# Optimization experiments

Hardware: AMD Instinct MI355X
Metric: run time of the kernel (lower is better)

Reference implementation:

```python
import jax, jax.numpy as jnp
import numpy as np

# Dims: B=4, T=4096, D=4096, G=1, C=4, K=128, I=4 (I2=2), M=32
B, T, D = 4, 4096, 4096
G, C, K, M = 1, 4, 128, 32
I = 4  # 2*dynamic_hidden_dim
EPS = 1e-6


def setup_inputs() -> dict:
    key = jax.random.key(0)
    k1, k2, k3, k4 = jax.random.split(key, 4)
    query_vec = jax.random.normal(k1, (B, T, D), dtype=jnp.float32)
    dw1 = jax.random.normal(k2, (D, G, C, K), dtype=jnp.float32) * 0.02
    qkw = jax.random.normal(k3, (G, C, K, I, M), dtype=jnp.float32) * 0.02
    dd_w = jax.random.normal(k4, (D, G, M * C), dtype=jnp.float32) * 0.02
    return {"query_vec": query_vec, "dw1": dw1, "qkw": qkw, "dd_w": dd_w}


def _rmsnorm_noscale(x):
    var = jnp.mean(jnp.square(x), axis=-1, keepdims=True)
    return x * jax.lax.rsqrt(var + EPS)


def reference(query_vec, dw1, qkw, dd_w):
    # dw_hidden: [B,T,G,C,K]
    dw_hidden = jnp.einsum('btd,dgck->btgck', query_vec, dw1)
    dw_hidden = jax.nn.gelu(dw_hidden, approximate=False)  # torch nn.GELU() = exact erf
    # w: [B,T,G,C,I,M]; split along I into w1,w2 of [B,T,G,C,I/2,M]
    w = jnp.einsum('btgck,gckim->btgcim', dw_hidden, qkw)
    w1, w2 = jnp.split(w, 2, axis=-2)
    w1 = _rmsnorm_noscale(w1)
    # unbind along C=4: order is (pre_q, pre_k, post_q, post_k)
    pre_qw1, pre_kw1, post_qw1, post_kw1 = (w1[:, :, :, i] for i in range(4))
    pre_qw2, pre_kw2, post_qw2, post_kw2 = (w2[:, :, :, i] for i in range(4))
    # dd: [B,T,G,4M] -> tanh -> split into 4 of [B,T,G,M]
    dd = jnp.tanh(jnp.einsum('btd,dgm->btgm', query_vec, dd_w))
    pre_qdd, pre_kdd, post_qdd, post_kdd = jnp.split(dd, 4, axis=-1)
    # gen_cache=True path: KW [B,T,2,M,M]
    eye = jnp.eye(M, dtype=query_vec.dtype)
    pre_kw = jnp.einsum('bsgim,bsgin->bsmn', pre_kw1, pre_kw2) + pre_kdd[:, :, 0, :, None] * eye
    post_kw = jnp.einsum('bsgim,bsgin->bsmn', post_kw1, post_kw2) + post_kdd[:, :, 0, :, None] * eye
    KW = jnp.stack((pre_kw, post_kw), axis=-3)
    return (pre_qw1, pre_qw2, pre_kw1, pre_kw2, pre_qdd, pre_kdd,
            post_qw1, post_qw2, post_kw1, post_kw2, post_qdd, post_kdd, KW)
```

## Files before the change

kernel.cpp:

```cpp
#include <hip/hip_runtime.h>
#include <hip/hip_bf16.h>


typedef _Float16 half8 __attribute__((ext_vector_type(8)));
typedef float f32x4 __attribute__((ext_vector_type(4)));

#define BT_TOK 16384
#define DDIM   4096

static constexpr int OFF_PRE_QW1  = 0;
static constexpr int OFF_PRE_QW2  = 1048576;
static constexpr int OFF_PRE_KW1  = 2097152;
static constexpr int OFF_PRE_KW2  = 3145728;
static constexpr int OFF_PRE_QDD  = 4194304;
static constexpr int OFF_PRE_KDD  = 4718592;
static constexpr int OFF_POST_QW1 = 5242880;
static constexpr int OFF_POST_QW2 = 6291456;
static constexpr int OFF_POST_KW1 = 7340032;
static constexpr int OFF_POST_KW2 = 8388608;
static constexpr int OFF_POST_QDD = 9437184;
static constexpr int OFF_POST_KDD = 9961472;
static constexpr int OFF_KW       = 10485760;

typedef __attribute__((address_space(3))) void lds_void;
typedef const __attribute__((address_space(1))) void gbl_void;

__device__ __forceinline__ void gload16(const void* g, void* l) {
  __builtin_amdgcn_global_load_lds((gbl_void*)g, (lds_void*)l, 16, 0, 0);
}

__global__ __launch_bounds__(256) void convert_a(const float* __restrict__ q,
                                                 _Float16* __restrict__ a) {
  const int stride = gridDim.x * blockDim.x;
  for (int i = blockIdx.x * blockDim.x + threadIdx.x; i < (BT_TOK * DDIM) / 8;
       i += stride) {
    const float4* p = (const float4*)(q + (size_t)i * 8);
    float4 x = p[0], y = p[1];
    half8 h;
    h[0] = (_Float16)x.x; h[1] = (_Float16)x.y;
    h[2] = (_Float16)x.z; h[3] = (_Float16)x.w;
    h[4] = (_Float16)y.x; h[5] = (_Float16)y.y;
    h[6] = (_Float16)y.z; h[7] = (_Float16)y.w;
    *(half8*)(a + (size_t)i * 8) = h;
  }
}

__global__ __launch_bounds__(256) void build_bt(const float* __restrict__ dw1,
                                                const float* __restrict__ ddw,
                                                _Float16* __restrict__ Bt) {
  __shared__ float tile[64][65];
  const int bn = blockIdx.x % 10, bd = blockIdx.x / 10;
  const int n0 = bn * 64, d0 = bd * 64;
  const int tid = threadIdx.x;
  const int ln = tid & 63;
  const int rr = tid >> 6;
#pragma unroll
  for (int i = 0; i < 16; ++i) {
    int dl = rr + i * 4;
    int d = d0 + dl, n = n0 + ln;
    float v = (n < 512) ? dw1[d * 512 + n] : ddw[d * 128 + (n - 512)];
    tile[dl][ln] = v;
  }
  __syncthreads();
#pragma unroll
  for (int i = 0; i < 16; ++i) {
    int nl = rr + i * 4;
    Bt[(size_t)(n0 + nl) * DDIM + d0 + ln] = (_Float16)tile[ln][nl];
  }
}

__global__ __launch_bounds__(256) void build_qkwT(const float* __restrict__ qkw,
                                                  _Float16* __restrict__ qT) {
  __shared__ float t[128][129];
  const int c = blockIdx.x;
  const float* src = qkw + c * 16384;
  for (int z = threadIdx.x; z < 16384; z += 256) {
    int k = z >> 7, n = z & 127;
    t[k][n] = src[z];
  }
  __syncthreads();
  for (int z = threadIdx.x; z < 16384; z += 256) {
    int n = z >> 7, k = z & 127;
    qT[c * 16384 + z] = (_Float16)t[k][n];
  }
}

__global__ __launch_bounds__(256) void gemm_main(const _Float16* __restrict__ A,
                                                 const _Float16* __restrict__ Bt,
                                                 _Float16* __restrict__ Hg,
                                                 float* __restrict__ out) {
  __shared__ _Float16 As[2][8192];
  __shared__ _Float16 Bs[2][8192];

  int wg = (int)blockIdx.x;
  wg = (wg & 7) * 80 + (wg >> 3);
  const int mtile = wg / 5, ntile = wg - mtile * 5;
  const int m0 = mtile << 7, n0 = ntile << 7;

  const int tid = threadIdx.x;
  const int wave = tid >> 6, lane = tid & 63;
  const int lq = lane >> 4, lc = lane & 15;

  int aoff[4], boff[4], lbase[4];
#pragma unroll
  for (int j = 0; j < 4; ++j) {
    int slot = j * 256 + wave * 64 + lane;
    int row = slot >> 3;
    int gs = (slot & 7) ^ (row & 7);
    aoff[j] = (m0 + row) * DDIM + gs * 8;
    boff[j] = (n0 + row) * DDIM + gs * 8;
    lbase[j] = j * 2048 + wave * 512;
  }
  const int wm = (wave >> 1) << 6, wn = (wave & 1) << 6;

  f32x4 acc[4][4];
#pragma unroll
  for (int i = 0; i < 4; ++i)
#pragma unroll
    for (int j = 0; j < 4; ++j) acc[i][j] = f32x4{0.f, 0.f, 0.f, 0.f};

  auto stage = [&](int b, int k0) {
#pragma unroll
    for (int j = 0; j < 4; ++j) gload16(A + aoff[j] + k0, &As[b][lbase[j]]);
#pragma unroll
    for (int j = 0; j < 4; ++j) gload16(Bt + boff[j] + k0, &Bs[b][lbase[j]]);
  };

  auto compute = [&](int b) {
#pragma unroll
    for (int kk = 0; kk < 2; ++kk) {
      half8 af[4], bf[4];
      const int kb = kk * 4 + lq;
#pragma unroll
      for (int f = 0; f < 4; ++f) {
        int rowA = wm + f * 16 + lc;
        af[f] = *(const half8*)(&As[b][rowA * 64 + ((kb ^ (rowA & 7)) << 3)]);
        int rowB = wn + f * 16 + lc;
        bf[f] = *(const half8*)(&Bs[b][rowB * 64 + ((kb ^ (rowB & 7)) << 3)]);
      }
#pragma unroll
      for (int mf = 0; mf < 4; ++mf)
#pragma unroll
        for (int nf = 0; nf < 4; ++nf)
          acc[mf][nf] = __builtin_amdgcn_mfma_f32_16x16x32_f16(
              af[mf], bf[nf], acc[mf][nf], 0, 0, 0);
    }
  };

  stage(0, 0);
  __syncthreads();
  for (int t = 0; t < 63; ++t) {
    stage((t + 1) & 1, (t + 1) << 6);
    compute(t & 1);
    __syncthreads();
  }
  compute(1);

  if (ntile < 4) {
#pragma unroll
    for (int mf = 0; mf < 4; ++mf)
#pragma unroll
      for (int nf = 0; nf < 4; ++nf)
#pragma unroll
        for (int r = 0; r < 4; ++r) {
          int row = m0 + wm + mf * 16 + lq * 4 + r;
          int col = n0 + wn + nf * 16 + lc;
          float v = acc[mf][nf][r];
          float g = 0.5f * v * (1.0f + erff(v * 0.70710678118654752f));
          Hg[(size_t)row * 512 + col] = (_Float16)g;
        }
  } else {
#pragma unroll
    for (int mf = 0; mf < 4; ++mf)
#pragma unroll
      for (int nf = 0; nf < 4; ++nf)
#pragma unroll
        for (int r = 0; r < 4; ++r) {
          int row = m0 + wm + mf * 16 + lq * 4 + r;
          int j = wn + nf * 16 + lc;
          int t = j >> 5;
          int base = (t & 2) ? ((t & 1) ? OFF_POST_KDD : OFF_POST_QDD)
                             : ((t & 1) ? OFF_PRE_KDD : OFF_PRE_QDD);
          out[base + row * 32 + (j & 31)] = tanhf(acc[mf][nf][r]);
        }
  }
}

__global__ __launch_bounds__(256) void epilogue_k(const _Float16* __restrict__ Hg,
                                                  const _Float16* __restrict__ qT,
                                                  float* __restrict__ out) {
  __shared__ _Float16 hga[16][520];
  __shared__ float stash[2][4][16][32];
  __shared__ float ddl[2][16][32];
  const int tid = threadIdx.x;
  const int wave = tid >> 6, lane = tid & 63;
  const int lq = lane >> 4, lc = lane & 15;
  const int tok0 = blockIdx.x * 16;
  const int c = wave;

#pragma unroll
  for (int z = 0; z < 4; ++z) {
    int flat = z * 256 + tid;
    int row = flat >> 6, c16 = flat & 63;
    *(half8*)(&hga[row][c16 * 8]) =
        *(const half8*)(Hg + (size_t)(tok0 + row) * 512 + c16 * 8);
  }

#pragma unroll
  for (int z = 0; z < 4; ++z) {
    int idx = z * 256 + tid;
    int pp = idx >> 9, tl = (idx >> 5) & 15, m = idx & 31;
    ddl[pp][tl][m] =
        out[(pp ? OFF_POST_KDD : OFF_PRE_KDD) + (tok0 + tl) * 32 + m];
  }
  __syncthreads();

  half8 af[4];
#pragma unroll
  for (int kf = 0; kf < 4; ++kf)
    af[kf] = *(const half8*)(&hga[lc][c * 128 + kf * 32 + lq * 8]);

  f32x4 acc[8];
#pragma unroll
  for (int nf = 0; nf < 8; ++nf) acc[nf] = f32x4{0.f, 0.f, 0.f, 0.f};
#pragma unroll
  for (int nf = 0; nf < 8; ++nf) {
    const _Float16* brow = qT + c * 16384 + (nf * 16 + lc) * 128 + lq * 8;
#pragma unroll
    for (int kf = 0; kf < 4; ++kf) {
      half8 bf = *(const half8*)(brow + kf * 32);
      acc[nf] = __builtin_amdgcn_mfma_f32_16x16x32_f16(af[kf], bf, acc[nf], 0, 0, 0);
    }
  }

  const int w1base = (c >> 1) * OFF_POST_QW1 + (c & 1) * OFF_PRE_KW1;
  const int w2base = w1base + OFF_PRE_QW2;
  const int cs = c >> 1;
  const bool isk = (c & 1);

#pragma unroll
  for (int i = 0; i < 4; ++i) {
    float vn0[4], vn1[4];
#pragma unroll
    for (int r = 0; r < 4; ++r) {
      vn0[r] = acc[2 * i][r];
      vn1[r] = acc[2 * i + 1][r];
    }
    if (i < 2) {
#pragma unroll
      for (int r = 0; r < 4; ++r) {
        float ss = vn0[r] * vn0[r] + vn1[r] * vn1[r];
        ss += __shfl_xor(ss, 1);
        ss += __shfl_xor(ss, 2);
        ss += __shfl_xor(ss, 4);
        ss += __shfl_xor(ss, 8);
        float sc = rsqrtf(ss * 0.03125f + 1e-6f);
        vn0[r] *= sc;
        vn1[r] *= sc;
      }
    }
    const int basei = ((i < 2) ? w1base : w2base) + (i & 1) * 32;
#pragma unroll
    for (int r = 0; r < 4; ++r) {
      int token = tok0 + lq * 4 + r;
      out[basei + token * 64 + lc] = vn0[r];
      out[basei + token * 64 + 16 + lc] = vn1[r];
      if (isk) {
        stash[cs][i][lq * 4 + r][lc] = vn0[r];
        stash[cs][i][lq * 4 + r][16 + lc] = vn1[r];
      }
    }
  }
  __syncthreads();

#pragma unroll 8
  for (int it = 0; it < 128; ++it) {
    int flat = it * 256 + tid;
    int pp = flat >> 14, rest = flat & 16383;
    int tl = rest >> 10, mrow = (rest >> 5) & 31, n = rest & 31;
    float v = stash[pp][0][tl][mrow] * stash[pp][2][tl][n] +
              stash[pp][1][tl][mrow] * stash[pp][3][tl][n];
    if (mrow == n) v += ddl[pp][tl][n];
    out[OFF_KW + (tok0 + tl) * 2048 + pp * 1024 + mrow * 32 + n] = v;
  }
}

extern "C" void kernel_launch(void* const* d_in, const int* in_sizes, int n_in,
                              void* d_out, int out_size, void* d_ws, size_t ws_size,
                              hipStream_t stream) {
  const float* q   = (const float*)d_in[0];
  const float* dw1 = (const float*)d_in[1];
  const float* qkw = (const float*)d_in[2];
  const float* ddw = (const float*)d_in[3];
  float* out = (float*)d_out;

  _Float16* Ah = (_Float16*)d_ws;
  _Float16* Bt = Ah + (size_t)BT_TOK * DDIM;
  _Float16* Hg = Bt + (size_t)640 * DDIM;
  _Float16* qT = Hg + (size_t)BT_TOK * 512;

  convert_a<<<2048, 256, 0, stream>>>(q, Ah);
  build_bt<<<640, 256, 0, stream>>>(dw1, ddw, Bt);
  build_qkwT<<<4, 256, 0, stream>>>(qkw, qT);
  gemm_main<<<640, 256, 0, stream>>>(Ah, Bt, Hg, out);
  epilogue_k<<<1024, 256, 0, stream>>>(Hg, qT, out);
}
```

Measured before the change: 667.8 us.

## Retile GEMM to 128x160 tiles, add MFMA priority, vectorize KW stores

The main GEMM now uses 128x160 output tiles (4 N-tiles covering 640 columns), so it launches 512 workgroups instead of 640. This cuts A-matrix reloads, since each A tile is read 4 times instead of 5, and the wave count now matches 256 CUs more evenly. It also raises wave priority around the MFMA blocks, and the epilogue picks the GELU or tanh path per column instead of per tile. The KW outer-product epilogue now writes float4 vectors, reducing store instruction count. The cost is more accumulator registers and more LDS per block, which may lower occupancy.

```diff
diff --git a/kernel.cpp b/kernel.cpp
--- a/kernel.cpp
+++ b/kernel.cpp
@@ -90,60 +90,69 @@
                                                  _Float16* __restrict__ Hg,
                                                  float* __restrict__ out) {
   __shared__ _Float16 As[2][8192];
-  __shared__ _Float16 Bs[2][8192];
+  __shared__ _Float16 Bs[2][10240];
 
   int wg = (int)blockIdx.x;
-  wg = (wg & 7) * 80 + (wg >> 3);
-  const int mtile = wg / 5, ntile = wg - mtile * 5;
-  const int m0 = mtile << 7, n0 = ntile << 7;
+  wg = (wg & 7) * 64 + (wg >> 3);
+  const int mtile = wg >> 2, ntile = wg & 3;
+  const int m0 = mtile << 7, n0 = ntile * 160;
 
   const int tid = threadIdx.x;
   const int wave = tid >> 6, lane = tid & 63;
   const int lq = lane >> 4, lc = lane & 15;
 
-  int aoff[4], boff[4], lbase[4];
-#pragma unroll
-  for (int j = 0; j < 4; ++j) {
+  int aoff[4], boff[5], lbA[4], lbB[5];
+#pragma unroll
+  for (int j = 0; j < 5; ++j) {
     int slot = j * 256 + wave * 64 + lane;
     int row = slot >> 3;
     int gs = (slot & 7) ^ (row & 7);
-    aoff[j] = (m0 + row) * DDIM + gs * 8;
+    if (j < 4) {
+      aoff[j] = (m0 + row) * DDIM + gs * 8;
+      lbA[j] = j * 2048 + wave * 512;
+    }
     boff[j] = (n0 + row) * DDIM + gs * 8;
-    lbase[j] = j * 2048 + wave * 512;
-  }
-  const int wm = (wave >> 1) << 6, wn = (wave & 1) << 6;
-
-  f32x4 acc[4][4];
+    lbB[j] = j * 2048 + wave * 512;
+  }
+  const int wm = (wave >> 1) << 6;
+  const int wn = (wave & 1) * 80;
+
+  f32x4 acc[4][5];
 #pragma unroll
   for (int i = 0; i < 4; ++i)
 #pragma unroll
-    for (int j = 0; j < 4; ++j) acc[i][j] = f32x4{0.f, 0.f, 0.f, 0.f};
+    for (int j = 0; j < 5; ++j) acc[i][j] = f32x4{0.f, 0.f, 0.f, 0.f};
 
   auto stage = [&](int b, int k0) {
 #pragma unroll
-    for (int j = 0; j < 4; ++j) gload16(A + aoff[j] + k0, &As[b][lbase[j]]);
-#pragma unroll
-    for (int j = 0; j < 4; ++j) gload16(Bt + boff[j] + k0, &Bs[b][lbase[j]]);
+    for (int j = 0; j < 4; ++j) gload16(A + aoff[j] + k0, &As[b][lbA[j]]);
+#pragma unroll
+    for (int j = 0; j < 5; ++j) gload16(Bt + boff[j] + k0, &Bs[b][lbB[j]]);
   };
 
   auto compute = [&](int b) {
 #pragma unroll
     for (int kk = 0; kk < 2; ++kk) {
-      half8 af[4], bf[4];
+      half8 af[4], bf[5];
       const int kb = kk * 4 + lq;
 #pragma unroll
       for (int f = 0; f < 4; ++f) {
         int rowA = wm + f * 16 + lc;
         af[f] = *(const half8*)(&As[b][rowA * 64 + ((kb ^ (rowA & 7)) << 3)]);
+      }
+#pragma unroll
+      for (int f = 0; f < 5; ++f) {
         int rowB = wn + f * 16 + lc;
         bf[f] = *(const half8*)(&Bs[b][rowB * 64 + ((kb ^ (rowB & 7)) << 3)]);
       }
+      __builtin_amdgcn_s_setprio(1);
 #pragma unroll
       for (int mf = 0; mf < 4; ++mf)
 #pragma unroll
-        for (int nf = 0; nf < 4; ++nf)
+        for (int nf = 0; nf < 5; ++nf)
           acc[mf][nf] = __builtin_amdgcn_mfma_f32_16x16x32_f16(
               af[mf], bf[nf], acc[mf][nf], 0, 0, 0);
+      __builtin_amdgcn_s_setprio(0);
     }
   };
 
@@ -156,34 +165,29 @@
   }
   compute(1);
 
-  if (ntile < 4) {
-#pragma unroll
-    for (int mf = 0; mf < 4; ++mf)
-#pragma unroll
-      for (int nf = 0; nf < 4; ++nf)
+#pragma unroll
+  for (int mf = 0; mf < 4; ++mf)
+#pragma unroll
+    for (int nf = 0; nf < 5; ++nf) {
+      int colg = n0 + wn + nf * 16 + lc;
+      int row0 = m0 + wm + mf * 16 + lq * 4;
+      if (colg < 512) {
 #pragma unroll
         for (int r = 0; r < 4; ++r) {
-          int row = m0 + wm + mf * 16 + lq * 4 + r;
-          int col = n0 + wn + nf * 16 + lc;
           float v = acc[mf][nf][r];
           float g = 0.5f * v * (1.0f + erff(v * 0.70710678118654752f));
-          Hg[(size_t)row * 512 + col] = (_Float16)g;
+          Hg[(size_t)(row0 + r) * 512 + colg] = (_Float16)g;
         }
-  } else {
-#pragma unroll
-    for (int mf = 0; mf < 4; ++mf)
-#pragma unroll
-      for (int nf = 0; nf < 4; ++nf)
-#pragma unroll
-        for (int r = 0; r < 4; ++r) {
-          int row = m0 + wm + mf * 16 + lq * 4 + r;
-          int j = wn + nf * 16 + lc;
-          int t = j >> 5;
-          int base = (t & 2) ? ((t & 1) ? OFF_POST_KDD : OFF_POST_QDD)
-                             : ((t & 1) ? OFF_PRE_KDD : OFF_PRE_QDD);
-          out[base + row * 32 + (j & 31)] = tanhf(acc[mf][nf][r]);
-        }
-  }
+      } else {
+        int j = colg - 512;
+        int t = j >> 5;
+        int base = (t & 2) ? ((t & 1) ? OFF_POST_KDD : OFF_POST_QDD)
+                           : ((t & 1) ? OFF_PRE_KDD : OFF_PRE_QDD);
+#pragma unroll
+        for (int r = 0; r < 4; ++r)
+          out[base + (row0 + r) * 32 + (j & 31)] = tanhf(acc[mf][nf][r]);
+      }
+    }
 }
 
 __global__ __launch_bounds__(256) void epilogue_k(const _Float16* __restrict__ Hg,
@@ -274,14 +278,17 @@
   __syncthreads();
 
 #pragma unroll 8
-  for (int it = 0; it < 128; ++it) {
+  for (int it = 0; it < 32; ++it) {
     int flat = it * 256 + tid;
-    int pp = flat >> 14, rest = flat & 16383;
-    int tl = rest >> 10, mrow = (rest >> 5) & 31, n = rest & 31;
-    float v = stash[pp][0][tl][mrow] * stash[pp][2][tl][n] +
-              stash[pp][1][tl][mrow] * stash[pp][3][tl][n];
-    if (mrow == n) v += ddl[pp][tl][n];
-    out[OFF_KW + (tok0 + tl) * 2048 + pp * 1024 + mrow * 32 + n] = v;
+    int pp = flat >> 12, rest = flat & 4095;
+    int tl = rest >> 8, mrow = (rest >> 3) & 31, n4 = (flat & 7) * 4;
+    f32x4 s2 = *(const f32x4*)(&stash[pp][2][tl][n4]);
+    f32x4 s3 = *(const f32x4*)(&stash[pp][3][tl][n4]);
+    float a0 = stash[pp][0][tl][mrow];
+    float a1 = stash[pp][1][tl][mrow];
+    f32x4 v = a0 * s2 + a1 * s3;
+    if ((mrow >> 2) == (flat & 7)) v[mrow & 3] += ddl[pp][tl][mrow];
+    *(f32x4*)(&out[OFF_KW + (tok0 + tl) * 2048 + pp * 1024 + mrow * 32 + n4]) = v;
   }
 }
 
@@ -302,6 +309,6 @@
   convert_a<<<2048, 256, 0, stream>>>(q, Ah);
   build_bt<<<640, 256, 0, stream>>>(dw1, ddw, Bt);
   build_qkwT<<<4, 256, 0, stream>>>(qkw, qT);
-  gemm_main<<<640, 256, 0, stream>>>(Ah, Bt, Hg, out);
+  gemm_main<<<512, 256, 0, stream>>>(Ah, Bt, Hg, out);
   epilogue_k<<<1024, 256, 0, stream>>>(Hg, qT, out);
 }
```

New measurement: 695.2 us. 1.04x slower.

## Fuse second einsum, rmsnorm and KW into main GEMM with 3-stage pipeline

Applied to the files above, without the earlier changes.

The main GEMM now runs with 512 threads and a triple-buffered LDS pipeline using explicit vmcnt waits and setprio. Its GELU tile stays in LDS and feeds the qkw projection, rmsnorm and KW outer products in the same kernel, so the Hg intermediate no longer makes a round trip through global memory. A separate epilogue launch is also removed. The diagonal kdd add moves into a small extra kernel, since the kdd values come from a different workgroup. Risks include higher LDS use (96KB) limiting occupancy, and a KW write/read ordering dependency across kernels.

```diff
diff --git a/kernel.cpp b/kernel.cpp
--- a/kernel.cpp
+++ b/kernel.cpp
@@ -51,15 +51,12 @@
   __shared__ float tile[64][65];
   const int bn = blockIdx.x % 10, bd = blockIdx.x / 10;
   const int n0 = bn * 64, d0 = bd * 64;
-  const int tid = threadIdx.x;
-  const int ln = tid & 63;
-  const int rr = tid >> 6;
+  const int ln = threadIdx.x & 63, rr = threadIdx.x >> 6;
 #pragma unroll
   for (int i = 0; i < 16; ++i) {
     int dl = rr + i * 4;
     int d = d0 + dl, n = n0 + ln;
-    float v = (n < 512) ? dw1[d * 512 + n] : ddw[d * 128 + (n - 512)];
-    tile[dl][ln] = v;
+    tile[dl][ln] = (n < 512) ? dw1[d * 512 + n] : ddw[d * 128 + (n - 512)];
   }
   __syncthreads();
 #pragma unroll
@@ -85,12 +82,12 @@
   }
 }
 
-__global__ __launch_bounds__(256) void gemm_main(const _Float16* __restrict__ A,
-                                                 const _Float16* __restrict__ Bt,
-                                                 _Float16* __restrict__ Hg,
-                                                 float* __restrict__ out) {
-  __shared__ _Float16 As[2][8192];
-  __shared__ _Float16 Bs[2][8192];
+__global__ __launch_bounds__(512) void gemm_fused(const _Float16* __restrict__ A,
+                                                  const _Float16* __restrict__ Bt,
+                                                  const _Float16* __restrict__ qT,
+                                                  float* __restrict__ out) {
+  __shared__ __align__(16) char lds_raw[98304];
+  _Float16* lh = (_Float16*)lds_raw;
 
   int wg = (int)blockIdx.x;
   wg = (wg & 7) * 80 + (wg >> 3);
@@ -100,189 +97,191 @@
   const int tid = threadIdx.x;
   const int wave = tid >> 6, lane = tid & 63;
   const int lq = lane >> 4, lc = lane & 15;
-
-  int aoff[4], boff[4], lbase[4];
-#pragma unroll
-  for (int j = 0; j < 4; ++j) {
-    int slot = j * 256 + wave * 64 + lane;
+  const int wm = (wave >> 1) << 5;
+  const int wn = (wave & 1) << 6;
+
+  int aoff[2], boff[2], lb[2];
+#pragma unroll
+  for (int j = 0; j < 2; ++j) {
+    int slot = j * 512 + tid;
     int row = slot >> 3;
     int gs = (slot & 7) ^ (row & 7);
     aoff[j] = (m0 + row) * DDIM + gs * 8;
     boff[j] = (n0 + row) * DDIM + gs * 8;
-    lbase[j] = j * 2048 + wave * 512;
-  }
-  const int wm = (wave >> 1) << 6, wn = (wave & 1) << 6;
-
-  f32x4 acc[4][4];
-#pragma unroll
-  for (int i = 0; i < 4; ++i)
+    lb[j] = j * 4096 + wave * 512;
+  }
+
+  f32x4 acc[2][4];
+#pragma unroll
+  for (int i = 0; i < 2; ++i)
 #pragma unroll
     for (int j = 0; j < 4; ++j) acc[i][j] = f32x4{0.f, 0.f, 0.f, 0.f};
 
-  auto stage = [&](int b, int k0) {
-#pragma unroll
-    for (int j = 0; j < 4; ++j) gload16(A + aoff[j] + k0, &As[b][lbase[j]]);
-#pragma unroll
-    for (int j = 0; j < 4; ++j) gload16(Bt + boff[j] + k0, &Bs[b][lbase[j]]);
+  auto stage = [&](int kt) {
+    int b = kt % 3;
+#pragma unroll
+    for (int j = 0; j < 2; ++j)
+      gload16(A + aoff[j] + kt * 64, lh + b * 8192 + lb[j]);
+#pragma unroll
+    for (int j = 0; j < 2; ++j)
+      gload16(Bt + boff[j] + kt * 64, lh + 24576 + b * 8192 + lb[j]);
   };
 
-  auto compute = [&](int b) {
+  auto compute = [&](int kt) {
+    const _Float16* Ab = lh + (kt % 3) * 8192;
+    const _Float16* Bb = lh + 24576 + (kt % 3) * 8192;
 #pragma unroll
     for (int kk = 0; kk < 2; ++kk) {
-      half8 af[4], bf[4];
+      half8 af[2], bf[4];
       const int kb = kk * 4 + lq;
 #pragma unroll
+      for (int f = 0; f < 2; ++f) {
+        int rowA = wm + f * 16 + lc;
+        af[f] = *(const half8*)(Ab + rowA * 64 + ((kb ^ (rowA & 7)) << 3));
+      }
+#pragma unroll
       for (int f = 0; f < 4; ++f) {
-        int rowA = wm + f * 16 + lc;
-        af[f] = *(const half8*)(&As[b][rowA * 64 + ((kb ^ (rowA & 7)) << 3)]);
         int rowB = wn + f * 16 + lc;
-        bf[f] = *(const half8*)(&Bs[b][rowB * 64 + ((kb ^ (rowB & 7)) << 3)]);
-      }
-#pragma unroll
-      for (int mf = 0; mf < 4; ++mf)
+        bf[f] = *(const half8*)(Bb + rowB * 64 + ((kb ^ (rowB & 7)) << 3));
+      }
+      __builtin_amdgcn_s_setprio(1);
+#pragma unroll
+      for (int mf = 0; mf < 2; ++mf)
 #pragma unroll
         for (int nf = 0; nf < 4; ++nf)
           acc[mf][nf] = __builtin_amdgcn_mfma_f32_16x16x32_f16(
               af[mf], bf[nf], acc[mf][nf], 0, 0, 0);
+      __builtin_amdgcn_s_setprio(0);
     }
   };
 
-  stage(0, 0);
+  stage(0);
+  stage(1);
+  for (int t = 0; t < 64; ++t) {
+    if (t < 63) {
+      asm volatile("s_waitcnt vmcnt(4)" ::: "memory");
+    } else {
+      asm volatile("s_waitcnt vmcnt(0)" ::: "memory");
+    }
+    __builtin_amdgcn_s_barrier();
+    __builtin_amdgcn_sched_barrier(0);
+    if (t < 62) stage(t + 2);
+    compute(t);
+  }
   __syncthreads();
-  for (int t = 0; t < 63; ++t) {
-    stage((t + 1) & 1, (t + 1) << 6);
-    compute(t & 1);
-    __syncthreads();
-  }
-  compute(1);
-
-  if (ntile < 4) {
-#pragma unroll
-    for (int mf = 0; mf < 4; ++mf)
+
+  const int c = ntile;
+  if (c < 4) {
+#pragma unroll
+    for (int mf = 0; mf < 2; ++mf)
 #pragma unroll
       for (int nf = 0; nf < 4; ++nf)
 #pragma unroll
         for (int r = 0; r < 4; ++r) {
-          int row = m0 + wm + mf * 16 + lq * 4 + r;
-          int col = n0 + wn + nf * 16 + lc;
+          int row = wm + mf * 16 + lq * 4 + r;
+          int col = wn + nf * 16 + lc;
           float v = acc[mf][nf][r];
           float g = 0.5f * v * (1.0f + erff(v * 0.70710678118654752f));
-          Hg[(size_t)row * 512 + col] = (_Float16)g;
+          lh[row * 136 + col] = (_Float16)g;
         }
+    __syncthreads();
+
+    half8 a2[4];
+#pragma unroll
+    for (int kf = 0; kf < 4; ++kf)
+      a2[kf] = *(const half8*)(lh + (wave * 16 + lc) * 136 + kf * 32 + lq * 8);
+    f32x4 acc2[8];
+#pragma unroll
+    for (int nf = 0; nf < 8; ++nf) acc2[nf] = f32x4{0.f, 0.f, 0.f, 0.f};
+#pragma unroll
+    for (int nf = 0; nf < 8; ++nf) {
+      const _Float16* brow = qT + c * 16384 + (nf * 16 + lc) * 128 + lq * 8;
+#pragma unroll
+      for (int kf = 0; kf < 4; ++kf) {
+        half8 b2 = *(const half8*)(brow + kf * 32);
+        acc2[nf] = __builtin_amdgcn_mfma_f32_16x16x32_f16(a2[kf], b2, acc2[nf], 0, 0, 0);
+      }
+    }
+    __syncthreads();
+
+    const int w1base = (c >> 1) * OFF_POST_QW1 + (c & 1) * OFF_PRE_KW1;
+    const int w2base = w1base + OFF_PRE_QW2;
+    const int tok0 = m0 + wave * 16;
+    float* st = (float*)lds_raw + wave * 2048;
+
+#pragma unroll
+    for (int i = 0; i < 4; ++i) {
+      float vn0[4], vn1[4];
+#pragma unroll
+      for (int r = 0; r < 4; ++r) {
+        vn0[r] = acc2[2 * i][r];
+        vn1[r] = acc2[2 * i + 1][r];
+      }
+      if (i < 2) {
+#pragma unroll
+        for (int r = 0; r < 4; ++r) {
+          float ss = vn0[r] * vn0[r] + vn1[r] * vn1[r];
+          ss += __shfl_xor(ss, 1);
+          ss += __shfl_xor(ss, 2);
+          ss += __shfl_xor(ss, 4);
+          ss += __shfl_xor(ss, 8);
+          float sc = rsqrtf(ss * 0.03125f + 1e-6f);
+          vn0[r] *= sc;
+          vn1[r] *= sc;
+        }
+      }
+      const int basei = ((i < 2) ? w1base : w2base) + (i & 1) * 32;
+#pragma unroll
+      for (int r = 0; r < 4; ++r) {
+        int token = tok0 + lq * 4 + r;
+        out[basei + token * 64 + lc] = vn0[r];
+        out[basei + token * 64 + 16 + lc] = vn1[r];
+        if (c & 1) {
+          st[i * 512 + (lq * 4 + r) * 32 + lc] = vn0[r];
+          st[i * 512 + (lq * 4 + r) * 32 + 16 + lc] = vn1[r];
+        }
+      }
+    }
+
+    if (c & 1) {
+      const int pp = c >> 1;
+#pragma unroll 8
+      for (int it = 0; it < 64; ++it) {
+        int slot = it * 64 + lane;
+        int tl = slot >> 8;
+        int mrow = (slot >> 3) & 31, n4 = (slot & 7) << 2;
+        f32x4 s2 = *(const f32x4*)(st + 2 * 512 + tl * 32 + n4);
+        f32x4 s3 = *(const f32x4*)(st + 3 * 512 + tl * 32 + n4);
+        float a0 = st[0 * 512 + tl * 32 + mrow];
+        float a1 = st[1 * 512 + tl * 32 + mrow];
+        f32x4 v = a0 * s2 + a1 * s3;
+        *(f32x4*)(&out[OFF_KW + (size_t)(tok0 + tl) * 2048 + pp * 1024 +
+                       mrow * 32 + n4]) = v;
+      }
+    }
   } else {
 #pragma unroll
-    for (int mf = 0; mf < 4; ++mf)
-#pragma unroll
-      for (int nf = 0; nf < 4; ++nf)
-#pragma unroll
-        for (int r = 0; r < 4; ++r) {
-          int row = m0 + wm + mf * 16 + lq * 4 + r;
-          int j = wn + nf * 16 + lc;
-          int t = j >> 5;
-          int base = (t & 2) ? ((t & 1) ? OFF_POST_KDD : OFF_POST_QDD)
-                             : ((t & 1) ? OFF_PRE_KDD : OFF_PRE_QDD);
-          out[base + row * 32 + (j & 31)] = tanhf(acc[mf][nf][r]);
-        }
-  }
-}
-
-__global__ __launch_bounds__(256) void epilogue_k(const _Float16* __restrict__ Hg,
-                                                  const _Float16* __restrict__ qT,
-                                                  float* __restrict__ out) {
-  __shared__ _Float16 hga[16][520];
-  __shared__ float stash[2][4][16][32];
-  __shared__ float ddl[2][16][32];
-  const int tid = threadIdx.x;
-  const int wave = tid >> 6, lane = tid & 63;
-  const int lq = lane >> 4, lc = lane & 15;
-  const int tok0 = blockIdx.x * 16;
-  const int c = wave;
-
-#pragma unroll
-  for (int z = 0; z < 4; ++z) {
-    int flat = z * 256 + tid;
-    int row = flat >> 6, c16 = flat & 63;
-    *(half8*)(&hga[row][c16 * 8]) =
-        *(const half8*)(Hg + (size_t)(tok0 + row) * 512 + c16 * 8);
-  }
-
-#pragma unroll
-  for (int z = 0; z < 4; ++z) {
-    int idx = z * 256 + tid;
-    int pp = idx >> 9, tl = (idx >> 5) & 15, m = idx & 31;
-    ddl[pp][tl][m] =
-        out[(pp ? OFF_POST_KDD : OFF_PRE_KDD) + (tok0 + tl) * 32 + m];
-  }
-  __syncthreads();
-
-  half8 af[4];
-#pragma unroll
-  for (int kf = 0; kf < 4; ++kf)
-    af[kf] = *(const half8*)(&hga[lc][c * 128 + kf * 32 + lq * 8]);
-
-  f32x4 acc[8];
-#pragma unroll
-  for (int nf = 0; nf < 8; ++nf) acc[nf] = f32x4{0.f, 0.f, 0.f, 0.f};
-#pragma unroll
-  for (int nf = 0; nf < 8; ++nf) {
-    const _Float16* brow = qT + c * 16384 + (nf * 16 + lc) * 128 + lq * 8;
-#pragma unroll
-    for (int kf = 0; kf < 4; ++kf) {
-      half8 bf = *(const half8*)(brow + kf * 32);
-      acc[nf] = __builtin_amdgcn_mfma_f32_16x16x32_f16(af[kf], bf, acc[nf], 0, 0, 0);
-    }
-  }
-
-  const int w1base = (c >> 1) * OFF_POST_QW1 + (c & 1) * OFF_PRE_KW1;
-  const int w2base = w1base + OFF_PRE_QW2;
-  const int cs = c >> 1;
-  const bool isk = (c & 1);
-
-#pragma unroll
-  for (int i = 0; i < 4; ++i) {
-    float vn0[4], vn1[4];
-#pragma unroll
-    for (int r = 0; r < 4; ++r) {
-      vn0[r] = acc[2 * i][r];
-      vn1[r] = acc[2 * i + 1][r];
-    }
-    if (i < 2) {
-#pragma unroll
-      for (int r = 0; r < 4; ++r) {
-        float ss = vn0[r] * vn0[r] + vn1[r] * vn1[r];
-        ss += __shfl_xor(ss, 1);
-        ss += __shfl_xor(ss, 2);
-        ss += __shfl_xor(ss, 4);
-        ss += __shfl_xor(ss, 8);
-        float sc = rsqrtf(ss * 0.03125f + 1e-6f);
-        vn0[r] *= sc;
-        vn1[r] *= sc;
-      }
-    }
-    const int basei = ((i < 2) ? w1base : w2base) + (i & 1) * 32;
-#pragma unroll
-    for (int r = 0; r < 4; ++r) {
-      int token = tok0 + lq * 4 + r;
-      out[basei + token * 64 + lc] = vn0[r];
-      out[basei + token * 64 + 16 + lc] = vn1[r];
-      if (isk) {
-        stash[cs][i][lq * 4 + r][lc] = vn0[r];
-        stash[cs][i][lq * 4 + r][16 + lc] = vn1[r];
-      }
-    }
-  }
-  __syncthreads();
-
-#pragma unroll 8
-  for (int it = 0; it < 128; ++it) {
-    int flat = it * 256 + tid;
-    int pp = flat >> 14, rest = flat & 16383;
-    int tl = rest >> 10, mrow = (rest >> 5) & 31, n = rest & 31;
-    float v = stash[pp][0][tl][mrow] * stash[pp][2][tl][n] +
-              stash[pp][1][tl][mrow] * stash[pp][3][tl][n];
-    if (mrow == n) v += ddl[pp][tl][n];
-    out[OFF_KW + (tok0 + tl) * 2048 + pp * 1024 + mrow * 32 + n] = v;
-  }
+    for (int mf = 0; mf < 2; ++mf)
+#pragma unroll
+      for (int nf = 0; nf < 4; ++nf) {
+        int j = wn + nf * 16 + lc;
+        int t = j >> 5;
+        int base = (t & 2) ? ((t & 1) ? OFF_POST_KDD : OFF_POST_QDD)
+                           : ((t & 1) ? OFF_PRE_KDD : OFF_PRE_QDD);
+        int row0 = m0 + wm + mf * 16 + lq * 4;
+#pragma unroll
+        for (int r = 0; r < 4; ++r)
+          out[base + (row0 + r) * 32 + (j & 31)] = tanhf(acc[mf][nf][r]);
+      }
+  }
+}
+
+__global__ __launch_bounds__(256) void kw_diag(float* __restrict__ out) {
+  int idx = blockIdx.x * 256 + threadIdx.x;
+  int tok = idx >> 6;
+  int pp = (idx >> 5) & 1, m = idx & 31;
+  float kdd = out[(pp ? OFF_POST_KDD : OFF_PRE_KDD) + tok * 32 + m];
+  out[OFF_KW + (size_t)tok * 2048 + pp * 1024 + m * 33] += kdd;
 }
 
 extern "C" void kernel_launch(void* const* d_in, const int* in_sizes, int n_in,
@@ -296,12 +295,11 @@
 
   _Float16* Ah = (_Float16*)d_ws;
   _Float16* Bt = Ah + (size_t)BT_TOK * DDIM;
-  _Float16* Hg = Bt + (size_t)640 * DDIM;
-  _Float16* qT = Hg + (size_t)BT_TOK * 512;
+  _Float16* qT = Bt + (size_t)640 * DDIM;
 
   convert_a<<<2048, 256, 0, stream>>>(q, Ah);
   build_bt<<<640, 256, 0, stream>>>(dw1, ddw, Bt);
   build_qkwT<<<4, 256, 0, stream>>>(qkw, qT);
-  gemm_main<<<640, 256, 0, stream>>>(Ah, Bt, Hg, out);
-  epilogue_k<<<1024, 256, 0, stream>>>(Hg, qT, out);
-}
+  gemm_fused<<<640, 512, 0, stream>>>(Ah, Bt, qT, out);
+  kw_diag<<<4096, 256, 0, stream>>>(out);
+}
```

Measured after the change: 639.7 us. 4.2% less time.
